# Kernel optimization log

Hardware: AMD Instinct MI355X
Metric: run time of the kernel (lower is better)

The kernel has to match this reference:

```python
import jax, jax.numpy as jnp
import numpy as np

L, N, I, H = 512, 512, 128, 128

def setup_inputs() -> dict:
    key = jax.random.key(0)
    ks = jax.random.split(key, 6)
    inp = {
        'input': jax.random.normal(ks[0], (L, N, I), dtype=jnp.float32),
        'hc': jnp.zeros((N, 2 * H), dtype=jnp.float32),
        'is_initial': jax.random.randint(ks[1], (L, N), 0, 2, dtype=jnp.int32),
        'W_ih': jax.random.normal(ks[2], (4 * H, I), dtype=jnp.float32) * (1.0 / np.sqrt(H)),
        'W_hh': jax.random.normal(ks[3], (4 * H, H), dtype=jnp.float32) * (1.0 / np.sqrt(H)),
        'b_ih': jax.random.normal(ks[4], (4 * H,), dtype=jnp.float32) * 0.01,
        'b_hh': jax.random.normal(ks[5], (4 * H,), dtype=jnp.float32) * 0.01,
    }
    return inp

def reference(input, hc, is_initial, W_ih, W_hh, b_ih, b_hh):
    h0, c0 = jnp.split(hc, 2, axis=-1)                 # [N,H] each
    mask = 1.0 - is_initial.astype(input.dtype)        # [L,N]; 0 where episode resets

    def step(carry, xm):
        h, c = carry
        x, m = xm                                      # x:[N,I], m:[N]
        h = h * m[:, None]
        c = c * m[:, None]
        # PyTorch LSTMCell gate order: i, f, g, o
        gates = x @ W_ih.T + b_ih + h @ W_hh.T + b_hh  # [N,4H]
        i_g, f_g, g_g, o_g = jnp.split(gates, 4, axis=-1)
        i_g = jax.nn.sigmoid(i_g)
        f_g = jax.nn.sigmoid(f_g)
        g_g = jnp.tanh(g_g)
        o_g = jax.nn.sigmoid(o_g)
        c = f_g * c + i_g * g_g
        h = o_g * jnp.tanh(c)
        return (h, c), h

    (h, c), outputs = jax.lax.scan(step, (h0, c0), (input, mask))
    # final hc: cat([h,c],-1) is [N,2H]; with N==L the expand(L,-1) is a no-op
    hc_out = jnp.broadcast_to(jnp.concatenate([h, c], axis=-1), (L, 2 * H))
    return outputs, hc_out
```

## Files before the change

### kernel.cpp

```cpp
#include <hip/hip_runtime.h>
#include <hip/hip_fp16.h>
#include <stdint.h>

#define LT 512
#define NB 512
#define DI 128
#define DH 128
#define G4 512
#define MROWS (LT * NB)

typedef _Float16 f16;
typedef __attribute__((ext_vector_type(2))) _Float16 f16x2;
typedef __attribute__((ext_vector_type(8))) _Float16 f16x8;
typedef __attribute__((ext_vector_type(4))) float floatx4;

__device__ __forceinline__ float dot2f(uint32_t a, uint32_t b, float c) {
#if __has_builtin(__builtin_amdgcn_fdot2)
    return __builtin_amdgcn_fdot2(__builtin_bit_cast(f16x2, a),
                                  __builtin_bit_cast(f16x2, b), c, false);
#else
    f16x2 pa = __builtin_bit_cast(f16x2, a);
    f16x2 pb = __builtin_bit_cast(f16x2, b);
    return c + (float)pa.x * (float)pb.x + (float)pa.y * (float)pb.y;
#endif
}

__device__ __forceinline__ uint32_t pack2(float x, float y) {
    f16x2 p;
    p.x = (_Float16)x;
    p.y = (_Float16)y;
    return __builtin_bit_cast(uint32_t, p);
}

__device__ __forceinline__ float sigm(float v) {
    return 1.f / (1.f + __expf(-v));
}

__device__ __forceinline__ float tanh_(float v) {
    float a = fabsf(v);
    float e = __expf(-2.f * a);
    float r = (1.f - e) / (1.f + e);
    return v < 0.f ? -r : r;
}

__launch_bounds__(512, 4)
__global__ void gemm_xgates(const float* __restrict__ x,
                            const float* __restrict__ Wih,
                            const float* __restrict__ bih,
                            const float* __restrict__ bhh,
                            f16* __restrict__ gx)
{
    __shared__ uint4 wx[128 * 16];
    const int tid = threadIdx.x;
    const size_t rowbase = (size_t)blockIdx.x * 128;

    {
        const float4* src = (const float4*)(x + rowbase * DI) + (size_t)tid * 8;
#pragma unroll
        for (int i = 0; i < 4; ++i) {
            float4 a = src[2 * i];
            float4 b = src[2 * i + 1];
            uint4 u;
            u.x = pack2(a.x, a.y); u.y = pack2(a.z, a.w);
            u.z = pack2(b.x, b.y); u.w = pack2(b.z, b.w);
            int flat = tid * 4 + i;
            int row  = flat >> 4;
            int m    = flat & 15;
            wx[row * 16 + (m ^ (row & 15))] = u;
        }
    }

    const int lane = tid & 63;
    const int w    = tid >> 6;
    const int l16  = lane & 15;
    const int quad = lane >> 4;
    const int j    = w * 16 + l16;

    f16x8 bfrag[4][4];
    float bs[4];
#pragma unroll
    for (int gs = 0; gs < 4; ++gs) {
        int gate = gs * 128 + j;
        bs[gs] = bih[gate] + bhh[gate];
        const float4* wp = (const float4*)(Wih + (size_t)gate * DI);
#pragma unroll
        for (int kc = 0; kc < 4; ++kc) {
            float4 a = wp[kc * 8 + quad * 2];
            float4 b = wp[kc * 8 + quad * 2 + 1];
            uint4 u;
            u.x = pack2(a.x, a.y); u.y = pack2(a.z, a.w);
            u.z = pack2(b.x, b.y); u.w = pack2(b.z, b.w);
            bfrag[gs][kc] = __builtin_bit_cast(f16x8, u);
        }
    }
    __syncthreads();

    uint2* gp = (uint2*)gx;
#pragma unroll
    for (int rs = 0; rs < 8; ++rs) {
        f16x8 afrag[4];
        int row = rs * 16 + l16;
#pragma unroll
        for (int kc = 0; kc < 4; ++kc) {
            int m = kc * 4 + quad;
            afrag[kc] = __builtin_bit_cast(f16x8, wx[row * 16 + (m ^ (row & 15))]);
        }
        floatx4 acc[4];
#pragma unroll
        for (int gs = 0; gs < 4; ++gs)
            acc[gs] = (floatx4){bs[gs], bs[gs], bs[gs], bs[gs]};
#pragma unroll
        for (int kc = 0; kc < 4; ++kc) {
#pragma unroll
            for (int gs = 0; gs < 4; ++gs)
                acc[gs] = __builtin_amdgcn_mfma_f32_16x16x32_f16(
                    afrag[kc], bfrag[gs][kc], acc[gs], 0, 0, 0);
        }
        size_t orow = rowbase + (size_t)rs * 16 + quad * 4;
#pragma unroll
        for (int r = 0; r < 4; ++r) {
            uint2 u;
            u.x = pack2(acc[0][r], acc[1][r]);
            u.y = pack2(acc[2][r], acc[3][r]);
            gp[(orow + r) * 128 + j] = u;
        }
    }
}

__launch_bounds__(512, 2)
__global__ void lstm_rec_mfma(const f16* __restrict__ gx,
                              const float* __restrict__ hc0,
                              const int*   __restrict__ isini,
                              const float* __restrict__ Whh,
                              float* __restrict__ out)
{
    const int tid  = threadIdx.x;
    const int lane = tid & 63;
    const int w    = tid >> 6;
    const int l16  = lane & 15;
    const int quad = lane >> 4;
    const int n0   = blockIdx.x * 2;
    const int j    = w * 16 + l16;

    __shared__ __align__(16) f16 sh_h[2][2][DH];
    __shared__ float sh_m[2][LT];

    for (int t = tid; t < LT; t += 512) {
        sh_m[0][t] = 1.f - (float)isini[(size_t)t * NB + n0];
        sh_m[1][t] = 1.f - (float)isini[(size_t)t * NB + n0 + 1];
    }

    f16x8 bfrag[4][4];
#pragma unroll
    for (int gs = 0; gs < 4; ++gs) {
        const float4* wp = (const float4*)(Whh + (size_t)(gs * 128 + j) * DH);
#pragma unroll
        for (int kc = 0; kc < 4; ++kc) {
            float4 a = wp[kc * 8 + quad * 2];
            float4 b = wp[kc * 8 + quad * 2 + 1];
            uint4 u;
            u.x = pack2(a.x, a.y); u.y = pack2(a.z, a.w);
            u.z = pack2(b.x, b.y); u.w = pack2(b.z, b.w);
            bfrag[gs][kc] = __builtin_bit_cast(f16x8, u);
        }
    }

    const bool act = (quad & 1) == 0;
    const int  nr  = quad >> 1;
    const int  n   = n0 + nr;

    float cval = 0.f, hval = 0.f;
    if (act) {
        hval = hc0[(size_t)n * (2 * DH) + j];
        cval = hc0[(size_t)n * (2 * DH) + DH + j];
        sh_h[0][nr][j] = (f16)hval;
    }

    const uint2* gxp = (const uint2*)gx;
    uint2 gxv = make_uint2(0u, 0u);
    if (act) gxv = gxp[(size_t)n * DH + j];
    __syncthreads();

    const int rowsel = l16 >> 3;
    float* outp = out + (size_t)n * DH + j;

    for (int t = 0; t < LT; ++t) {
        const int buf = t & 1;

        int tn = (t + 1 < LT) ? (t + 1) : t;
        uint2 gxn = make_uint2(0u, 0u);
        if (act) gxn = gxp[((size_t)tn * NB + n) * DH + j];

        const uint4* hb = (const uint4*)&sh_h[buf][0][0];
        floatx4 acc[4];
#pragma unroll
        for (int gs = 0; gs < 4; ++gs) acc[gs] = (floatx4){0.f, 0.f, 0.f, 0.f};
#pragma unroll
        for (int kc = 0; kc < 4; ++kc) {
            f16x8 af = __builtin_bit_cast(f16x8, hb[rowsel * 16 + kc * 4 + quad]);
#pragma unroll
            for (int gs = 0; gs < 4; ++gs)
                acc[gs] = __builtin_amdgcn_mfma_f32_16x16x32_f16(
                    af, bfrag[gs][kc], acc[gs], 0, 0, 0);
        }

        if (act) {
            const float m = sh_m[nr][t];
            f16x2 p01 = __builtin_bit_cast(f16x2, gxv.x);
            f16x2 p23 = __builtin_bit_cast(f16x2, gxv.y);
            float ig = (float)p01.x + m * acc[0][0];
            float fg = (float)p01.y + m * acc[1][0];
            float gg = (float)p23.x + m * acc[2][0];
            float og = (float)p23.y + m * acc[3][0];
            float cc = sigm(fg) * (m * cval) + sigm(ig) * tanh_(gg);
            hval = sigm(og) * tanh_(cc);
            cval = cc;
            outp[(size_t)t * (NB * DH)] = hval;
            sh_h[buf ^ 1][nr][j] = (f16)hval;
        }
        gxv = gxn;
        __syncthreads();
    }

    if (act) {
        size_t base = (size_t)LT * NB * DH;
        out[base + (size_t)n * (2 * DH) + j]      = hval;
        out[base + (size_t)n * (2 * DH) + DH + j] = cval;
    }
}

__launch_bounds__(512, 2)
__global__ void lstm_fused(const float* __restrict__ x,
                           const float* __restrict__ hc0,
                           const int*   __restrict__ isini,
                           const float* __restrict__ Wih,
                           const float* __restrict__ Whh,
                           const float* __restrict__ bih,
                           const float* __restrict__ bhh,
                           float* __restrict__ out)
{
    const int g   = threadIdx.x;
    const int n0  = blockIdx.x * 2;

    __shared__ __align__(16) f16   sh_h[2][DH];
    __shared__ __align__(16) f16   sh_x[2][2][DI];
    __shared__ __align__(16) float sh_gates[2][G4];

    uint32_t wih[64], whh[64];
    {
        const float4* wi = (const float4*)(Wih + (size_t)g * DI);
        const float4* wh = (const float4*)(Whh + (size_t)g * DI);
#pragma unroll
        for (int i = 0; i < 32; ++i) {
            float4 a = wi[i];
            wih[2 * i]     = pack2(a.x, a.y);
            wih[2 * i + 1] = pack2(a.z, a.w);
            float4 b = wh[i];
            whh[2 * i]     = pack2(b.x, b.y);
            whh[2 * i + 1] = pack2(b.z, b.w);
        }
    }
    const float bias = bih[g] + bhh[g];
    const int row = (threadIdx.x >> 7) & 1;
    const int j   = threadIdx.x & 127;
    const int n   = n0 + row;

    float cval = 0.f, hval = 0.f;

    if (threadIdx.x < 256) {
        cval = hc0[(size_t)n * (2 * DH) + DH + j];
        float h0 = hc0[(size_t)n * (2 * DH) + j];
        sh_h[row][j] = (f16)h0;
    } else {
        float xv0 = x[((size_t)0 * NB + n) * DI + j];
        sh_x[0][row][j] = (f16)xv0;
    }
    __syncthreads();

    for (int t = 0; t < LT; ++t) {
        const float m0 = 1.f - (float)isini[(size_t)t * NB + n0];
        const float m1 = 1.f - (float)isini[(size_t)t * NB + n0 + 1];

        float xpre = 0.f;
        if (threadIdx.x >= 256) {
            int tp = (t + 1 < LT) ? (t + 1) : (LT - 1);
            xpre = x[((size_t)tp * NB + n) * DI + j];
        }

        const uint4* xp0 = (const uint4*)&sh_x[t & 1][0][0];
        const uint4* xp1 = (const uint4*)&sh_x[t & 1][1][0];
        const uint4* hp0 = (const uint4*)&sh_h[0][0];
        const uint4* hp1 = (const uint4*)&sh_h[1][0];

        float ax0 = 0.f, ax0b = 0.f, ah0 = 0.f, ah0b = 0.f;
        float ax1 = 0.f, ax1b = 0.f, ah1 = 0.f, ah1b = 0.f;
#pragma unroll
        for (int i = 0; i < 16; ++i) {
            uint4 xv0 = xp0[i];
            uint4 xv1 = xp1[i];
            uint4 hv0 = hp0[i];
            uint4 hv1 = hp1[i];
            ax0  = dot2f(xv0.x, wih[4 * i + 0], ax0);
            ax0b = dot2f(xv0.y, wih[4 * i + 1], ax0b);
            ax0  = dot2f(xv0.z, wih[4 * i + 2], ax0);
            ax0b = dot2f(xv0.w, wih[4 * i + 3], ax0b);
            ah0  = dot2f(hv0.x, whh[4 * i + 0], ah0);
            ah0b = dot2f(hv0.y, whh[4 * i + 1], ah0b);
            ah0  = dot2f(hv0.z, whh[4 * i + 2], ah0);
            ah0b = dot2f(hv0.w, whh[4 * i + 3], ah0b);
            ax1  = dot2f(xv1.x, wih[4 * i + 0], ax1);
            ax1b = dot2f(xv1.y, wih[4 * i + 1], ax1b);
            ax1  = dot2f(xv1.z, wih[4 * i + 2], ax1);
            ax1b = dot2f(xv1.w, wih[4 * i + 3], ax1b);
            ah1  = dot2f(hv1.x, whh[4 * i + 0], ah1);
            ah1b = dot2f(hv1.y, whh[4 * i + 1], ah1b);
            ah1  = dot2f(hv1.z, whh[4 * i + 2], ah1);
            ah1b = dot2f(hv1.w, whh[4 * i + 3], ah1b);
        }
        sh_gates[0][g] = bias + (ax0 + ax0b) + m0 * (ah0 + ah0b);
        sh_gates[1][g] = bias + (ax1 + ax1b) + m1 * (ah1 + ah1b);

        __syncthreads();

        if (threadIdx.x < 256) {
            float ig = sh_gates[row][j];
            float fg = sh_gates[row][128 + j];
            float gg = sh_gates[row][256 + j];
            float og = sh_gates[row][384 + j];
            float m  = row ? m1 : m0;
            float cc = m * cval;
            cc   = sigm(fg) * cc + sigm(ig) * tanh_(gg);
            hval = sigm(og) * tanh_(cc);
            cval = cc;
            out[((size_t)t * NB + n) * DH + j] = hval;
            sh_h[row][j] = (f16)hval;
        } else {
            sh_x[(t + 1) & 1][row][j] = (f16)xpre;
        }
        __syncthreads();
    }

    if (threadIdx.x < 256) {
        size_t base = (size_t)LT * NB * DH;
        out[base + (size_t)n * (2 * DH) + j]      = hval;
        out[base + (size_t)n * (2 * DH) + DH + j] = cval;
    }
}

extern "C" void kernel_launch(void* const* d_in, const int* in_sizes, int n_in,
                              void* d_out, int out_size, void* d_ws, size_t ws_size,
                              hipStream_t stream) {
    const float* x     = (const float*)d_in[0];
    const float* hc0   = (const float*)d_in[1];
    const int*   isini = (const int*)d_in[2];
    const float* Wih   = (const float*)d_in[3];
    const float* Whh   = (const float*)d_in[4];
    const float* bih   = (const float*)d_in[5];
    const float* bhh   = (const float*)d_in[6];
    float* out = (float*)d_out;

    const size_t need = (size_t)MROWS * G4 * sizeof(f16);
    if (ws_size >= need) {
        f16* gx = (f16*)d_ws;
        gemm_xgates<<<dim3(MROWS / 128), dim3(512), 0, stream>>>(x, Wih, bih, bhh, gx);
        lstm_rec_mfma<<<dim3(NB / 2), dim3(512), 0, stream>>>(gx, hc0, isini, Whh, out);
    } else {
        lstm_fused<<<dim3(NB / 2), dim3(512), 0, stream>>>(
            x, hc0, isini, Wih, Whh, bih, bhh, out);
    }
}
```

Baseline: 667.3 us.

## Fuse input projection into recurrent MFMA kernel, dropping gx workspace GEMM

Removes the separate input-projection GEMM and its f16 gate workspace. The recurrent kernel now concatenates x_t and masked h into one K=256 shared-memory row and does both projections with MFMA each step, prefetching x two steps ahead. The mask is folded into h before it is stored, and the divides in sigmoid and tanh become hardware reciprocals. This avoids writing and re-reading a large intermediate in exchange for twice the MFMA work per serial step and more weight registers.

```diff
diff --git a/kernel.cpp b/kernel.cpp
--- a/kernel.cpp
+++ b/kernel.cpp
@@ -6,24 +6,13 @@
 #define NB 512
 #define DI 128
 #define DH 128
-#define G4 512
-#define MROWS (LT * NB)
+#define AROW 272
+#define ASTR 34
 
 typedef _Float16 f16;
 typedef __attribute__((ext_vector_type(2))) _Float16 f16x2;
 typedef __attribute__((ext_vector_type(8))) _Float16 f16x8;
 typedef __attribute__((ext_vector_type(4))) float floatx4;
-
-__device__ __forceinline__ float dot2f(uint32_t a, uint32_t b, float c) {
-#if __has_builtin(__builtin_amdgcn_fdot2)
-    return __builtin_amdgcn_fdot2(__builtin_bit_cast(f16x2, a),
-                                  __builtin_bit_cast(f16x2, b), c, false);
-#else
-    f16x2 pa = __builtin_bit_cast(f16x2, a);
-    f16x2 pb = __builtin_bit_cast(f16x2, b);
-    return c + (float)pa.x * (float)pb.x + (float)pa.y * (float)pb.y;
-#endif
-}
 
 __device__ __forceinline__ uint32_t pack2(float x, float y) {
     f16x2 p;
@@ -32,107 +21,34 @@
     return __builtin_bit_cast(uint32_t, p);
 }
 
+__device__ __forceinline__ float frcp(float x) {
+#if __has_builtin(__builtin_amdgcn_rcpf)
+    return __builtin_amdgcn_rcpf(x);
+#else
+    return 1.f / x;
+#endif
+}
+
 __device__ __forceinline__ float sigm(float v) {
-    return 1.f / (1.f + __expf(-v));
+    return frcp(1.f + __expf(-v));
 }
 
 __device__ __forceinline__ float tanh_(float v) {
     float a = fabsf(v);
     float e = __expf(-2.f * a);
-    float r = (1.f - e) / (1.f + e);
+    float r = (1.f - e) * frcp(1.f + e);
     return v < 0.f ? -r : r;
 }
 
-__launch_bounds__(512, 4)
-__global__ void gemm_xgates(const float* __restrict__ x,
-                            const float* __restrict__ Wih,
-                            const float* __restrict__ bih,
-                            const float* __restrict__ bhh,
-                            f16* __restrict__ gx)
-{
-    __shared__ uint4 wx[128 * 16];
-    const int tid = threadIdx.x;
-    const size_t rowbase = (size_t)blockIdx.x * 128;
-
-    {
-        const float4* src = (const float4*)(x + rowbase * DI) + (size_t)tid * 8;
-#pragma unroll
-        for (int i = 0; i < 4; ++i) {
-            float4 a = src[2 * i];
-            float4 b = src[2 * i + 1];
-            uint4 u;
-            u.x = pack2(a.x, a.y); u.y = pack2(a.z, a.w);
-            u.z = pack2(b.x, b.y); u.w = pack2(b.z, b.w);
-            int flat = tid * 4 + i;
-            int row  = flat >> 4;
-            int m    = flat & 15;
-            wx[row * 16 + (m ^ (row & 15))] = u;
-        }
-    }
-
-    const int lane = tid & 63;
-    const int w    = tid >> 6;
-    const int l16  = lane & 15;
-    const int quad = lane >> 4;
-    const int j    = w * 16 + l16;
-
-    f16x8 bfrag[4][4];
-    float bs[4];
-#pragma unroll
-    for (int gs = 0; gs < 4; ++gs) {
-        int gate = gs * 128 + j;
-        bs[gs] = bih[gate] + bhh[gate];
-        const float4* wp = (const float4*)(Wih + (size_t)gate * DI);
-#pragma unroll
-        for (int kc = 0; kc < 4; ++kc) {
-            float4 a = wp[kc * 8 + quad * 2];
-            float4 b = wp[kc * 8 + quad * 2 + 1];
-            uint4 u;
-            u.x = pack2(a.x, a.y); u.y = pack2(a.z, a.w);
-            u.z = pack2(b.x, b.y); u.w = pack2(b.z, b.w);
-            bfrag[gs][kc] = __builtin_bit_cast(f16x8, u);
-        }
-    }
-    __syncthreads();
-
-    uint2* gp = (uint2*)gx;
-#pragma unroll
-    for (int rs = 0; rs < 8; ++rs) {
-        f16x8 afrag[4];
-        int row = rs * 16 + l16;
-#pragma unroll
-        for (int kc = 0; kc < 4; ++kc) {
-            int m = kc * 4 + quad;
-            afrag[kc] = __builtin_bit_cast(f16x8, wx[row * 16 + (m ^ (row & 15))]);
-        }
-        floatx4 acc[4];
-#pragma unroll
-        for (int gs = 0; gs < 4; ++gs)
-            acc[gs] = (floatx4){bs[gs], bs[gs], bs[gs], bs[gs]};
-#pragma unroll
-        for (int kc = 0; kc < 4; ++kc) {
-#pragma unroll
-            for (int gs = 0; gs < 4; ++gs)
-                acc[gs] = __builtin_amdgcn_mfma_f32_16x16x32_f16(
-                    afrag[kc], bfrag[gs][kc], acc[gs], 0, 0, 0);
-        }
-        size_t orow = rowbase + (size_t)rs * 16 + quad * 4;
-#pragma unroll
-        for (int r = 0; r < 4; ++r) {
-            uint2 u;
-            u.x = pack2(acc[0][r], acc[1][r]);
-            u.y = pack2(acc[2][r], acc[3][r]);
-            gp[(orow + r) * 128 + j] = u;
-        }
-    }
-}
-
 __launch_bounds__(512, 2)
-__global__ void lstm_rec_mfma(const f16* __restrict__ gx,
-                              const float* __restrict__ hc0,
-                              const int*   __restrict__ isini,
-                              const float* __restrict__ Whh,
-                              float* __restrict__ out)
+__global__ void lstm_fused_mfma(const float* __restrict__ x,
+                                const float* __restrict__ hc0,
+                                const int*   __restrict__ isini,
+                                const float* __restrict__ Wih,
+                                const float* __restrict__ Whh,
+                                const float* __restrict__ bih,
+                                const float* __restrict__ bhh,
+                                float* __restrict__ out)
 {
     const int tid  = threadIdx.x;
     const int lane = tid & 63;
@@ -142,7 +58,7 @@
     const int n0   = blockIdx.x * 2;
     const int j    = w * 16 + l16;
 
-    __shared__ __align__(16) f16 sh_h[2][2][DH];
+    __shared__ __align__(16) f16 sh_a[2][2][AROW];
     __shared__ float sh_m[2][LT];
 
     for (int t = tid; t < LT; t += 512) {
@@ -150,18 +66,31 @@
         sh_m[1][t] = 1.f - (float)isini[(size_t)t * NB + n0 + 1];
     }
 
-    f16x8 bfrag[4][4];
+    f16x8 bfrag[4][8];
+    float bs[4];
 #pragma unroll
     for (int gs = 0; gs < 4; ++gs) {
-        const float4* wp = (const float4*)(Whh + (size_t)(gs * 128 + j) * DH);
+        const int gate = gs * 128 + j;
+        bs[gs] = bih[gate] + bhh[gate];
+        const float4* wi = (const float4*)(Wih + (size_t)gate * DI);
+        const float4* wh = (const float4*)(Whh + (size_t)gate * DH);
 #pragma unroll
         for (int kc = 0; kc < 4; ++kc) {
-            float4 a = wp[kc * 8 + quad * 2];
-            float4 b = wp[kc * 8 + quad * 2 + 1];
+            float4 a = wi[kc * 8 + quad * 2];
+            float4 b = wi[kc * 8 + quad * 2 + 1];
             uint4 u;
             u.x = pack2(a.x, a.y); u.y = pack2(a.z, a.w);
             u.z = pack2(b.x, b.y); u.w = pack2(b.z, b.w);
             bfrag[gs][kc] = __builtin_bit_cast(f16x8, u);
+        }
+#pragma unroll
+        for (int kc = 0; kc < 4; ++kc) {
+            float4 a = wh[kc * 8 + quad * 2];
+            float4 b = wh[kc * 8 + quad * 2 + 1];
+            uint4 u;
+            u.x = pack2(a.x, a.y); u.y = pack2(a.z, a.w);
+            u.z = pack2(b.x, b.y); u.w = pack2(b.z, b.w);
+            bfrag[gs][4 + kc] = __builtin_bit_cast(f16x8, u);
         }
     }
 
@@ -169,178 +98,81 @@
     const int  nr  = quad >> 1;
     const int  n   = n0 + nr;
 
-    float cval = 0.f, hval = 0.f;
+    float cval = 0.f, hval = 0.f, mcur = 0.f;
     if (act) {
         hval = hc0[(size_t)n * (2 * DH) + j];
         cval = hc0[(size_t)n * (2 * DH) + DH + j];
-        sh_h[0][nr][j] = (f16)hval;
+        mcur = 1.f - (float)isini[n];
+        sh_a[0][nr][128 + j] = (f16)(hval * mcur);
     }
 
-    const uint2* gxp = (const uint2*)gx;
-    uint2 gxv = make_uint2(0u, 0u);
-    if (act) gxv = gxp[(size_t)n * DH + j];
+    const int  sflat = w * 8 + (lane & 7);
+    const int  srow  = sflat >> 5;
+    const int  sf4   = sflat & 31;
+    const bool sact  = (lane & 63) < 8;
+    float4 xp = {0.f, 0.f, 0.f, 0.f};
+    if (sact) {
+        const float4* sp0 = (const float4*)(x + ((size_t)0 * NB + n0 + srow) * DI);
+        float4 v = sp0[sf4];
+        uint2 u2;
+        u2.x = pack2(v.x, v.y); u2.y = pack2(v.z, v.w);
+        *(uint2*)&sh_a[0][srow][sf4 * 4] = u2;
+        const float4* sp1 = (const float4*)(x + ((size_t)1 * NB + n0 + srow) * DI);
+        xp = sp1[sf4];
+    }
     __syncthreads();
 
     const int rowsel = l16 >> 3;
     float* outp = out + (size_t)n * DH + j;
 
     for (int t = 0; t < LT; ++t) {
-        const int buf = t & 1;
+        const int buf  = t & 1;
+        const int nbuf = buf ^ 1;
 
-        int tn = (t + 1 < LT) ? (t + 1) : t;
-        uint2 gxn = make_uint2(0u, 0u);
-        if (act) gxn = gxp[((size_t)tn * NB + n) * DH + j];
+        const uint4* ab = (const uint4*)&sh_a[buf][0][0];
+        f16x8 af[8];
+#pragma unroll
+        for (int kc = 0; kc < 8; ++kc)
+            af[kc] = __builtin_bit_cast(f16x8, ab[rowsel * ASTR + kc * 4 + quad]);
 
-        const uint4* hb = (const uint4*)&sh_h[buf][0][0];
+        if (sact) {
+            uint2 u2;
+            u2.x = pack2(xp.x, xp.y); u2.y = pack2(xp.z, xp.w);
+            *(uint2*)&sh_a[nbuf][srow][sf4 * 4] = u2;
+            int t2 = (t + 2 < LT) ? (t + 2) : (LT - 1);
+            const float4* sp = (const float4*)(x + ((size_t)t2 * NB + n0 + srow) * DI);
+            xp = sp[sf4];
+        }
+
         floatx4 acc[4];
 #pragma unroll
         for (int gs = 0; gs < 4; ++gs) acc[gs] = (floatx4){0.f, 0.f, 0.f, 0.f};
 #pragma unroll
-        for (int kc = 0; kc < 4; ++kc) {
-            f16x8 af = __builtin_bit_cast(f16x8, hb[rowsel * 16 + kc * 4 + quad]);
+        for (int kc = 0; kc < 8; ++kc) {
 #pragma unroll
             for (int gs = 0; gs < 4; ++gs)
                 acc[gs] = __builtin_amdgcn_mfma_f32_16x16x32_f16(
-                    af, bfrag[gs][kc], acc[gs], 0, 0, 0);
+                    af[kc], bfrag[gs][kc], acc[gs], 0, 0, 0);
         }
 
         if (act) {
-            const float m = sh_m[nr][t];
-            f16x2 p01 = __builtin_bit_cast(f16x2, gxv.x);
-            f16x2 p23 = __builtin_bit_cast(f16x2, gxv.y);
-            float ig = (float)p01.x + m * acc[0][0];
-            float fg = (float)p01.y + m * acc[1][0];
-            float gg = (float)p23.x + m * acc[2][0];
-            float og = (float)p23.y + m * acc[3][0];
-            float cc = sigm(fg) * (m * cval) + sigm(ig) * tanh_(gg);
+            float ig = acc[0][0] + bs[0];
+            float fg = acc[1][0] + bs[1];
+            float gg = acc[2][0] + bs[2];
+            float og = acc[3][0] + bs[3];
+            float cc = sigm(fg) * (mcur * cval) + sigm(ig) * tanh_(gg);
             hval = sigm(og) * tanh_(cc);
             cval = cc;
             outp[(size_t)t * (NB * DH)] = hval;
-            sh_h[buf ^ 1][nr][j] = (f16)hval;
+            int t1 = (t + 1 < LT) ? (t + 1) : (LT - 1);
+            float mn = sh_m[nr][t1];
+            sh_a[nbuf][nr][128 + j] = (f16)(hval * mn);
+            mcur = mn;
         }
-        gxv = gxn;
         __syncthreads();
     }
 
     if (act) {
-        size_t base = (size_t)LT * NB * DH;
-        out[base + (size_t)n * (2 * DH) + j]      = hval;
-        out[base + (size_t)n * (2 * DH) + DH + j] = cval;
-    }
-}
-
-__launch_bounds__(512, 2)
-__global__ void lstm_fused(const float* __restrict__ x,
-                           const float* __restrict__ hc0,
-                           const int*   __restrict__ isini,
-                           const float* __restrict__ Wih,
-                           const float* __restrict__ Whh,
-                           const float* __restrict__ bih,
-                           const float* __restrict__ bhh,
-                           float* __restrict__ out)
-{
-    const int g   = threadIdx.x;
-    const int n0  = blockIdx.x * 2;
-
-    __shared__ __align__(16) f16   sh_h[2][DH];
-    __shared__ __align__(16) f16   sh_x[2][2][DI];
-    __shared__ __align__(16) float sh_gates[2][G4];
-
-    uint32_t wih[64], whh[64];
-    {
-        const float4* wi = (const float4*)(Wih + (size_t)g * DI);
-        const float4* wh = (const float4*)(Whh + (size_t)g * DI);
-#pragma unroll
-        for (int i = 0; i < 32; ++i) {
-            float4 a = wi[i];
-            wih[2 * i]     = pack2(a.x, a.y);
-            wih[2 * i + 1] = pack2(a.z, a.w);
-            float4 b = wh[i];
-            whh[2 * i]     = pack2(b.x, b.y);
-            whh[2 * i + 1] = pack2(b.z, b.w);
-        }
-    }
-    const float bias = bih[g] + bhh[g];
-    const int row = (threadIdx.x >> 7) & 1;
-    const int j   = threadIdx.x & 127;
-    const int n   = n0 + row;
-
-    float cval = 0.f, hval = 0.f;
-
-    if (threadIdx.x < 256) {
-        cval = hc0[(size_t)n * (2 * DH) + DH + j];
-        float h0 = hc0[(size_t)n * (2 * DH) + j];
-        sh_h[row][j] = (f16)h0;
-    } else {
-        float xv0 = x[((size_t)0 * NB + n) * DI + j];
-        sh_x[0][row][j] = (f16)xv0;
-    }
-    __syncthreads();
-
-    for (int t = 0; t < LT; ++t) {
-        const float m0 = 1.f - (float)isini[(size_t)t * NB + n0];
-        const float m1 = 1.f - (float)isini[(size_t)t * NB + n0 + 1];
-
-        float xpre = 0.f;
-        if (threadIdx.x >= 256) {
-            int tp = (t + 1 < LT) ? (t + 1) : (LT - 1);
-            xpre = x[((size_t)tp * NB + n) * DI + j];
-        }
-
-        const uint4* xp0 = (const uint4*)&sh_x[t & 1][0][0];
-        const uint4* xp1 = (const uint4*)&sh_x[t & 1][1][0];
-        const uint4* hp0 = (const uint4*)&sh_h[0][0];
-        const uint4* hp1 = (const uint4*)&sh_h[1][0];
-
-        float ax0 = 0.f, ax0b = 0.f, ah0 = 0.f, ah0b = 0.f;
-        float ax1 = 0.f, ax1b = 0.f, ah1 = 0.f, ah1b = 0.f;
-#pragma unroll
-        for (int i = 0; i < 16; ++i) {
-            uint4 xv0 = xp0[i];
-            uint4 xv1 = xp1[i];
-            uint4 hv0 = hp0[i];
-            uint4 hv1 = hp1[i];
-            ax0  = dot2f(xv0.x, wih[4 * i + 0], ax0);
-            ax0b = dot2f(xv0.y, wih[4 * i + 1], ax0b);
-            ax0  = dot2f(xv0.z, wih[4 * i + 2], ax0);
-            ax0b = dot2f(xv0.w, wih[4 * i + 3], ax0b);
-            ah0  = dot2f(hv0.x, whh[4 * i + 0], ah0);
-            ah0b = dot2f(hv0.y, whh[4 * i + 1], ah0b);
-            ah0  = dot2f(hv0.z, whh[4 * i + 2], ah0);
-            ah0b = dot2f(hv0.w, whh[4 * i + 3], ah0b);
-            ax1  = dot2f(xv1.x, wih[4 * i + 0], ax1);
-            ax1b = dot2f(xv1.y, wih[4 * i + 1], ax1b);
-            ax1  = dot2f(xv1.z, wih[4 * i + 2], ax1);
-            ax1b = dot2f(xv1.w, wih[4 * i + 3], ax1b);
-            ah1  = dot2f(hv1.x, whh[4 * i + 0], ah1);
-            ah1b = dot2f(hv1.y, whh[4 * i + 1], ah1b);
-            ah1  = dot2f(hv1.z, whh[4 * i + 2], ah1);
-            ah1b = dot2f(hv1.w, whh[4 * i + 3], ah1b);
-        }
-        sh_gates[0][g] = bias + (ax0 + ax0b) + m0 * (ah0 + ah0b);
-        sh_gates[1][g] = bias + (ax1 + ax1b) + m1 * (ah1 + ah1b);
-
-        __syncthreads();
-
-        if (threadIdx.x < 256) {
-            float ig = sh_gates[row][j];
-            float fg = sh_gates[row][128 + j];
-            float gg = sh_gates[row][256 + j];
-            float og = sh_gates[row][384 + j];
-            float m  = row ? m1 : m0;
-            float cc = m * cval;
-            cc   = sigm(fg) * cc + sigm(ig) * tanh_(gg);
-            hval = sigm(og) * tanh_(cc);
-            cval = cc;
-            out[((size_t)t * NB + n) * DH + j] = hval;
-            sh_h[row][j] = (f16)hval;
-        } else {
-            sh_x[(t + 1) & 1][row][j] = (f16)xpre;
-        }
-        __syncthreads();
-    }
-
-    if (threadIdx.x < 256) {
         size_t base = (size_t)LT * NB * DH;
         out[base + (size_t)n * (2 * DH) + j]      = hval;
         out[base + (size_t)n * (2 * DH) + DH + j] = cval;
@@ -359,13 +191,6 @@
     const float* bhh   = (const float*)d_in[6];
     float* out = (float*)d_out;
 
-    const size_t need = (size_t)MROWS * G4 * sizeof(f16);
-    if (ws_size >= need) {
-        f16* gx = (f16*)d_ws;
-        gemm_xgates<<<dim3(MROWS / 128), dim3(512), 0, stream>>>(x, Wih, bih, bhh, gx);
-        lstm_rec_mfma<<<dim3(NB / 2), dim3(512), 0, stream>>>(gx, hc0, isini, Whh, out);
-    } else {
-        lstm_fused<<<dim3(NB / 2), dim3(512), 0, stream>>>(
-            x, hc0, isini, Wih, Whh, bih, bhh, out);
-    }
+    lstm_fused_mfma<<<dim3(NB / 2), dim3(512), 0, stream>>>(
+        x, hc0, isini, Wih, Whh, bih, bhh, out);
 }
```

Measured after the change: 590.5 us. -11.5%, faster.
